# Kernel optimization log

Measured on AMD Instinct MI355X. Metric: run time of the kernel, lower is better.

The kernel has to match this reference:

```python
import jax, jax.numpy as jnp
import numpy as np

N, E, C, L = 50000, 800000, 64, 3  # nodes, edges, channels, message-passing layers
EPS = 1e-5  # torch.nn.LayerNorm default eps


def _mlp(h, W0, b0, W1, b1, W2, b2, g, beta):
    # MLP(input, hidden=[C, C], output=C) with ReLU between linears, LayerNorm at end
    h = jax.nn.relu(h @ W0 + b0)
    h = jax.nn.relu(h @ W1 + b1)
    h = h @ W2 + b2
    mu = jnp.mean(h, axis=-1, keepdims=True)
    var = jnp.var(h, axis=-1, keepdims=True)
    return (h - mu) * jax.lax.rsqrt(var + EPS) * g + beta


def setup_inputs() -> dict:
    key = jax.random.key(0)
    ks = jax.random.split(key, 12)
    def w(k, shape, fan_in):
        return (jax.random.normal(k, shape, jnp.float32) / np.float32(np.sqrt(fan_in)))
    return {
        "x": jax.random.normal(ks[0], (N, C), jnp.float32),
        "e": jax.random.normal(ks[1], (E, C), jnp.float32),
        "edge_index": jax.random.randint(ks[2], (2, E), 0, N),
        # edge_updater MLP params, stacked over L layers
        "ew0": w(ks[3], (L, 3 * C, C), 3 * C), "eb0": jnp.zeros((L, C), jnp.float32),
        "ew1": w(ks[4], (L, C, C), C),         "eb1": jnp.zeros((L, C), jnp.float32),
        "ew2": w(ks[5], (L, C, C), C),         "eb2": jnp.zeros((L, C), jnp.float32),
        "eg": jnp.ones((L, C), jnp.float32),   "ebt": jnp.zeros((L, C), jnp.float32),
        # node_updater MLP params
        "nw0": w(ks[6], (L, 2 * C, C), 2 * C), "nb0": jnp.zeros((L, C), jnp.float32),
        "nw1": w(ks[7], (L, C, C), C),         "nb1": jnp.zeros((L, C), jnp.float32),
        "nw2": w(ks[8], (L, C, C), C),         "nb2": jnp.zeros((L, C), jnp.float32),
        "ng": jnp.ones((L, C), jnp.float32),   "nbt": jnp.zeros((L, C), jnp.float32),
    }


def reference(x, e, edge_index, ew0, eb0, ew1, eb1, ew2, eb2, eg, ebt,
              nw0, nb0, nw1, nb1, nw2, nb2, ng, nbt):
    src, dst = edge_index[0], edge_index[1]
    for i in range(L):
        # e += edge_updater(cat(x_src, x_dst, e))
        e = e + _mlp(jnp.concatenate([x[src], x[dst], e], axis=1),
                     ew0[i], eb0[i], ew1[i], eb1[i], ew2[i], eb2[i], eg[i], ebt[i])
        # EdgeAggregation(aggr='add'): scatter-add edge features at target nodes
        agg = jax.ops.segment_sum(e, dst, num_segments=N)
        # x += node_updater(cat(x, agg))
        x = x + _mlp(jnp.concatenate([x, agg], axis=1),
                     nw0[i], nb0[i], nw1[i], nb1[i], nw2[i], nb2[i], ng[i], nbt[i])
    return (x, e)
```

## Files before the change

### kernel.cpp

```cpp
#include <hip/hip_runtime.h>

#define CH 64

using bf16x8 = __attribute__((ext_vector_type(8))) short;
using f32x4  = __attribute__((ext_vector_type(4))) float;

__device__ __forceinline__ unsigned short f2bf(float f) {
  unsigned int u = __float_as_uint(f);
  u = (u + 0x7FFFu + ((u >> 16) & 1u)) >> 16;
  return (unsigned short)u;
}

#define E0S 200
#define S64 72
#define N0S 136

#define EW0_L 0
#define EW1_L 12800
#define EW2_L 17408
#define EW_TOT 22016
#define EH0_L 22016
#define EH1_L 34816
#define E_LDS 39424

#define NW0_L 0
#define NW1_L 8704
#define NW2_L 13312
#define NW_TOT 17920
#define NH0_L 17920
#define NH1_L 26624
#define N_LDS 31232

#define WS_NW 66048
#define WS_AGG_B    262144
#define WS_ROWPTR_B 13062144
#define WS_NEXT_B   13262208
#define WS_EID_B    13462208

__global__ void prep_w(const float* __restrict__ ew0, const float* __restrict__ ew1,
                       const float* __restrict__ ew2, const float* __restrict__ nw0,
                       const float* __restrict__ nw1, const float* __restrict__ nw2,
                       unsigned short* __restrict__ ws) {
  int i = blockIdx.x * 256 + threadIdx.x;
  if (i < 36864) {
    int l = i / 12288, r = i % 12288, k = r / 64, n = r % 64;
    ws[l * EW_TOT + EW0_L + n * E0S + k] = f2bf(ew0[i]);
  } else if (i < 49152) {
    int j = i - 36864, l = j / 4096, r = j % 4096, k = r / 64, n = r % 64;
    ws[l * EW_TOT + EW1_L + n * S64 + k] = f2bf(ew1[j]);
  } else if (i < 61440) {
    int j = i - 49152, l = j / 4096, r = j % 4096, k = r / 64, n = r % 64;
    ws[l * EW_TOT + EW2_L + n * S64 + k] = f2bf(ew2[j]);
  } else if (i < 86016) {
    int j = i - 61440, l = j / 8192, r = j % 8192, k = r / 64, n = r % 64;
    ws[WS_NW + l * NW_TOT + NW0_L + n * N0S + k] = f2bf(nw0[j]);
  } else if (i < 98304) {
    int j = i - 86016, l = j / 4096, r = j % 4096, k = r / 64, n = r % 64;
    ws[WS_NW + l * NW_TOT + NW1_L + n * S64 + k] = f2bf(nw1[j]);
  } else if (i < 110592) {
    int j = i - 98304, l = j / 4096, r = j % 4096, k = r / 64, n = r % 64;
    ws[WS_NW + l * NW_TOT + NW2_L + n * S64 + k] = f2bf(nw2[j]);
  }
}

__global__ void hist_k(const int* __restrict__ dst, int* __restrict__ counts, int nE) {
  int i = blockIdx.x * 256 + threadIdx.x;
  if (i < nE) atomicAdd(counts + dst[i], 1);
}

__global__ void scan_k(const int* __restrict__ counts, int* __restrict__ row_ptr,
                       int* __restrict__ next, int n) {
  __shared__ int wsum[16];
  __shared__ int chunk_tot;
  __shared__ int base_sh;
  const int tid = threadIdx.x, lane = tid & 63, wv = tid >> 6;
  if (tid == 0) { base_sh = 0; row_ptr[0] = 0; }
  __syncthreads();
  for (int start = 0; start < n; start += 4096) {
    int idx = start + tid * 4;
    int v[4], s = 0;
#pragma unroll
    for (int k = 0; k < 4; ++k) { v[k] = (idx + k < n) ? counts[idx + k] : 0; s += v[k]; }
    int incl = s;
#pragma unroll
    for (int off = 1; off < 64; off <<= 1) {
      int t = __shfl_up(incl, off, 64);
      if (lane >= off) incl += t;
    }
    if (lane == 63) wsum[wv] = incl;
    __syncthreads();
    if (wv == 0 && lane < 16) {
      int w = wsum[lane];
      int wincl = w;
#pragma unroll
      for (int off = 1; off < 16; off <<= 1) {
        int t = __shfl_up(wincl, off, 16);
        if (lane >= off) wincl += t;
      }
      if (lane == 15) chunk_tot = wincl;
      wsum[lane] = wincl - w;
    }
    __syncthreads();
    int run = base_sh + wsum[wv] + (incl - s);
#pragma unroll
    for (int k = 0; k < 4; ++k) {
      int i = idx + k;
      if (i < n) { next[i] = run; run += v[k]; row_ptr[i + 1] = run; }
    }
    __syncthreads();
    if (tid == 0) base_sh += chunk_tot;
    __syncthreads();
  }
}

__global__ void scatter_k(const int* __restrict__ dst, int* __restrict__ next,
                          int* __restrict__ eid, int nE) {
  int i = blockIdx.x * 256 + threadIdx.x;
  if (i < nE) {
    int p = atomicAdd(next + dst[i], 1);
    eid[p] = i;
  }
}

__global__ __launch_bounds__(256, 2)
void edge_kernel(const float* x, const float* e_in, float* e_out,
                 const int* __restrict__ src, const int* __restrict__ dst,
                 const unsigned short* __restrict__ wg,
                 const float* __restrict__ b0, const float* __restrict__ b1,
                 const float* __restrict__ b2, const float* __restrict__ gam,
                 const float* __restrict__ bet, int nE) {
  __shared__ unsigned short lds[E_LDS];
  const int tid = threadIdx.x;
  {
    const uint4* s = (const uint4*)wg;
    uint4* d4 = (uint4*)lds;
    for (int i = tid; i < EW_TOT / 8; i += 256) d4[i] = s[i];
  }
  __syncthreads();

  const int wave = tid >> 6, lane = tid & 63;
  const int quad = lane >> 4, l15 = lane & 15;
  const int h0o = EH0_L + wave * 3200;
  const int h1o = EH1_L + wave * 1152;

  float b0c[4], b1c[4], b2c[4], gc[4], btc[4];
#pragma unroll
  for (int j = 0; j < 4; ++j) {
    int col = j * 16 + l15;
    b0c[j] = b0[col]; b1c[j] = b1[col]; b2c[j] = b2[col];
    gc[j] = gam[col]; btc[j] = bet[col];
  }

  for (int base = blockIdx.x * 64; base < nE; base += gridDim.x * 64) {
    const int ebase = base + wave * 16;
#pragma unroll
    for (int p = 0; p < 4; ++p) {
      int el = p * 4 + quad;
      int eidx = ebase + el;
      int s = src[eidx], d = dst[eidx];
      float4 vs = *(const float4*)(x + (size_t)s * CH + l15 * 4);
      float4 vd = *(const float4*)(x + (size_t)d * CH + l15 * 4);
      float4 ve = *(const float4*)(e_in + (size_t)eidx * CH + l15 * 4);
      ushort4 us; us.x = f2bf(vs.x); us.y = f2bf(vs.y); us.z = f2bf(vs.z); us.w = f2bf(vs.w);
      ushort4 ud; ud.x = f2bf(vd.x); ud.y = f2bf(vd.y); ud.z = f2bf(vd.z); ud.w = f2bf(vd.w);
      ushort4 ue; ue.x = f2bf(ve.x); ue.y = f2bf(ve.y); ue.z = f2bf(ve.z); ue.w = f2bf(ve.w);
      *(ushort4*)(lds + h0o + el * E0S + l15 * 4)       = us;
      *(ushort4*)(lds + h0o + el * E0S + 64 + l15 * 4)  = ud;
      *(ushort4*)(lds + h0o + el * E0S + 128 + l15 * 4) = ue;
    }
    f32x4 acc0[4];
#pragma unroll
    for (int j = 0; j < 4; ++j) acc0[j] = (f32x4){0.f, 0.f, 0.f, 0.f};
#pragma unroll
    for (int t = 0; t < 6; ++t) {
      bf16x8 a = *(const bf16x8*)(lds + h0o + l15 * E0S + t * 32 + quad * 8);
#pragma unroll
      for (int j = 0; j < 4; ++j) {
        bf16x8 b = *(const bf16x8*)(lds + EW0_L + (j * 16 + l15) * E0S + t * 32 + quad * 8);
        acc0[j] = __builtin_amdgcn_mfma_f32_16x16x32_bf16(a, b, acc0[j], 0, 0, 0);
      }
    }
#pragma unroll
    for (int j = 0; j < 4; ++j) {
      int col = j * 16 + l15;
#pragma unroll
      for (int r = 0; r < 4; ++r) {
        float v = fmaxf(acc0[j][r] + b0c[j], 0.f);
        lds[h1o + (quad * 4 + r) * S64 + col] = f2bf(v);
      }
    }
    f32x4 acc1[4];
#pragma unroll
    for (int j = 0; j < 4; ++j) acc1[j] = (f32x4){0.f, 0.f, 0.f, 0.f};
#pragma unroll
    for (int t = 0; t < 2; ++t) {
      bf16x8 a = *(const bf16x8*)(lds + h1o + l15 * S64 + t * 32 + quad * 8);
#pragma unroll
      for (int j = 0; j < 4; ++j) {
        bf16x8 b = *(const bf16x8*)(lds + EW1_L + (j * 16 + l15) * S64 + t * 32 + quad * 8);
        acc1[j] = __builtin_amdgcn_mfma_f32_16x16x32_bf16(a, b, acc1[j], 0, 0, 0);
      }
    }
#pragma unroll
    for (int j = 0; j < 4; ++j) {
      int col = j * 16 + l15;
#pragma unroll
      for (int r = 0; r < 4; ++r) {
        float v = fmaxf(acc1[j][r] + b1c[j], 0.f);
        lds[h0o + (quad * 4 + r) * S64 + col] = f2bf(v);
      }
    }
    f32x4 acc2[4];
#pragma unroll
    for (int j = 0; j < 4; ++j) acc2[j] = (f32x4){0.f, 0.f, 0.f, 0.f};
#pragma unroll
    for (int t = 0; t < 2; ++t) {
      bf16x8 a = *(const bf16x8*)(lds + h0o + l15 * S64 + t * 32 + quad * 8);
#pragma unroll
      for (int j = 0; j < 4; ++j) {
        bf16x8 b = *(const bf16x8*)(lds + EW2_L + (j * 16 + l15) * S64 + t * 32 + quad * 8);
        acc2[j] = __builtin_amdgcn_mfma_f32_16x16x32_bf16(a, b, acc2[j], 0, 0, 0);
      }
    }
    float vv[4][4], s1[4], s2[4];
#pragma unroll
    for (int r = 0; r < 4; ++r) { s1[r] = 0.f; s2[r] = 0.f; }
#pragma unroll
    for (int j = 0; j < 4; ++j)
#pragma unroll
      for (int r = 0; r < 4; ++r) {
        float v = acc2[j][r] + b2c[j];
        vv[j][r] = v; s1[r] += v; s2[r] += v * v;
      }
#pragma unroll
    for (int m = 1; m < 16; m <<= 1)
#pragma unroll
      for (int r = 0; r < 4; ++r) {
        s1[r] += __shfl_xor(s1[r], m, 64);
        s2[r] += __shfl_xor(s2[r], m, 64);
      }
#pragma unroll
    for (int r = 0; r < 4; ++r) {
      int eidx = ebase + quad * 4 + r;
      float mean = s1[r] * 0.015625f;
      float var = s2[r] * 0.015625f - mean * mean;
      float rstd = rsqrtf(var + 1e-5f);
      const float* ein_row = e_in + (size_t)eidx * CH;
      float* eout_row = e_out + (size_t)eidx * CH;
#pragma unroll
      for (int j = 0; j < 4; ++j) {
        int col = j * 16 + l15;
        float y = (vv[j][r] - mean) * rstd * gc[j] + btc[j];
        eout_row[col] = ein_row[col] + y;
      }
    }
  }
}

__global__ __launch_bounds__(256)
void agg_kernel(const float* __restrict__ e, const int* __restrict__ row_ptr,
                const int* __restrict__ eid, float* __restrict__ agg, int nN) {
  int node = blockIdx.x * 4 + (threadIdx.x >> 6);
  int lane = threadIdx.x & 63;
  if (node >= nN) return;
  int r0 = row_ptr[node], r1 = row_ptr[node + 1];
  float s0 = 0.f, s1 = 0.f, s2 = 0.f, s3 = 0.f;
  int i = r0;
  for (; i + 4 <= r1; i += 4) {
    int e0 = eid[i], e1 = eid[i + 1], e2 = eid[i + 2], e3 = eid[i + 3];
    s0 += e[(size_t)e0 * CH + lane];
    s1 += e[(size_t)e1 * CH + lane];
    s2 += e[(size_t)e2 * CH + lane];
    s3 += e[(size_t)e3 * CH + lane];
  }
  for (; i < r1; ++i) s0 += e[(size_t)eid[i] * CH + lane];
  agg[(size_t)node * CH + lane] = (s0 + s1) + (s2 + s3);
}

__global__ __launch_bounds__(256, 2)
void node_kernel(const float* x_in, const float* __restrict__ agg_in,
                 const unsigned short* __restrict__ wg,
                 const float* __restrict__ b0, const float* __restrict__ b1,
                 const float* __restrict__ b2, const float* __restrict__ gam,
                 const float* __restrict__ bet, float* x_out, int nN) {
  __shared__ unsigned short lds[N_LDS];
  const int tid = threadIdx.x;
  {
    const uint4* s = (const uint4*)wg;
    uint4* d4 = (uint4*)lds;
    for (int i = tid; i < NW_TOT / 8; i += 256) d4[i] = s[i];
  }
  __syncthreads();

  const int wave = tid >> 6, lane = tid & 63;
  const int quad = lane >> 4, l15 = lane & 15;
  const int nbase = (blockIdx.x * 4 + wave) * 16;
  if (nbase >= nN) return;
  const int h0o = NH0_L + wave * 2176;
  const int h1o = NH1_L + wave * 1152;

  float b0c[4], b1c[4], b2c[4], gc[4], btc[4];
#pragma unroll
  for (int j = 0; j < 4; ++j) {
    int col = j * 16 + l15;
    b0c[j] = b0[col]; b1c[j] = b1[col]; b2c[j] = b2[col];
    gc[j] = gam[col]; btc[j] = bet[col];
  }

#pragma unroll
  for (int p = 0; p < 4; ++p) {
    int nl = p * 4 + quad;
    int node = nbase + nl;
    float4 vx = *(const float4*)(x_in + (size_t)node * CH + l15 * 4);
    float4 va = *(const float4*)(agg_in + (size_t)node * CH + l15 * 4);
    ushort4 ux; ux.x = f2bf(vx.x); ux.y = f2bf(vx.y); ux.z = f2bf(vx.z); ux.w = f2bf(vx.w);
    ushort4 ua; ua.x = f2bf(va.x); ua.y = f2bf(va.y); ua.z = f2bf(va.z); ua.w = f2bf(va.w);
    *(ushort4*)(lds + h0o + nl * N0S + l15 * 4)      = ux;
    *(ushort4*)(lds + h0o + nl * N0S + 64 + l15 * 4) = ua;
  }
  f32x4 acc0[4];
#pragma unroll
  for (int j = 0; j < 4; ++j) acc0[j] = (f32x4){0.f, 0.f, 0.f, 0.f};
#pragma unroll
  for (int t = 0; t < 4; ++t) {
    bf16x8 a = *(const bf16x8*)(lds + h0o + l15 * N0S + t * 32 + quad * 8);
#pragma unroll
    for (int j = 0; j < 4; ++j) {
      bf16x8 b = *(const bf16x8*)(lds + NW0_L + (j * 16 + l15) * N0S + t * 32 + quad * 8);
      acc0[j] = __builtin_amdgcn_mfma_f32_16x16x32_bf16(a, b, acc0[j], 0, 0, 0);
    }
  }
#pragma unroll
  for (int j = 0; j < 4; ++j) {
    int col = j * 16 + l15;
#pragma unroll
    for (int r = 0; r < 4; ++r) {
      float v = fmaxf(acc0[j][r] + b0c[j], 0.f);
      lds[h1o + (quad * 4 + r) * S64 + col] = f2bf(v);
    }
  }
  f32x4 acc1[4];
#pragma unroll
  for (int j = 0; j < 4; ++j) acc1[j] = (f32x4){0.f, 0.f, 0.f, 0.f};
#pragma unroll
  for (int t = 0; t < 2; ++t) {
    bf16x8 a = *(const bf16x8*)(lds + h1o + l15 * S64 + t * 32 + quad * 8);
#pragma unroll
    for (int j = 0; j < 4; ++j) {
      bf16x8 b = *(const bf16x8*)(lds + NW1_L + (j * 16 + l15) * S64 + t * 32 + quad * 8);
      acc1[j] = __builtin_amdgcn_mfma_f32_16x16x32_bf16(a, b, acc1[j], 0, 0, 0);
    }
  }
#pragma unroll
  for (int j = 0; j < 4; ++j) {
    int col = j * 16 + l15;
#pragma unroll
    for (int r = 0; r < 4; ++r) {
      float v = fmaxf(acc1[j][r] + b1c[j], 0.f);
      lds[h0o + (quad * 4 + r) * S64 + col] = f2bf(v);
    }
  }
  f32x4 acc2[4];
#pragma unroll
  for (int j = 0; j < 4; ++j) acc2[j] = (f32x4){0.f, 0.f, 0.f, 0.f};
#pragma unroll
  for (int t = 0; t < 2; ++t) {
    bf16x8 a = *(const bf16x8*)(lds + h0o + l15 * S64 + t * 32 + quad * 8);
#pragma unroll
    for (int j = 0; j < 4; ++j) {
      bf16x8 b = *(const bf16x8*)(lds + NW2_L + (j * 16 + l15) * S64 + t * 32 + quad * 8);
      acc2[j] = __builtin_amdgcn_mfma_f32_16x16x32_bf16(a, b, acc2[j], 0, 0, 0);
    }
  }
  float vv[4][4], s1[4], s2[4];
#pragma unroll
  for (int r = 0; r < 4; ++r) { s1[r] = 0.f; s2[r] = 0.f; }
#pragma unroll
  for (int j = 0; j < 4; ++j)
#pragma unroll
    for (int r = 0; r < 4; ++r) {
      float v = acc2[j][r] + b2c[j];
      vv[j][r] = v; s1[r] += v; s2[r] += v * v;
    }
#pragma unroll
  for (int m = 1; m < 16; m <<= 1)
#pragma unroll
    for (int r = 0; r < 4; ++r) {
      s1[r] += __shfl_xor(s1[r], m, 64);
      s2[r] += __shfl_xor(s2[r], m, 64);
    }
#pragma unroll
  for (int r = 0; r < 4; ++r) {
    int node = nbase + quad * 4 + r;
    float mean = s1[r] * 0.015625f;
    float var = s2[r] * 0.015625f - mean * mean;
    float rstd = rsqrtf(var + 1e-5f);
    const float* xin_row = x_in + (size_t)node * CH;
    float* xout_row = x_out + (size_t)node * CH;
#pragma unroll
    for (int j = 0; j < 4; ++j) {
      int col = j * 16 + l15;
      float y = (vv[j][r] - mean) * rstd * gc[j] + btc[j];
      xout_row[col] = xin_row[col] + y;
    }
  }
}

extern "C" void kernel_launch(void* const* d_in, const int* in_sizes, int n_in,
                              void* d_out, int out_size, void* d_ws, size_t ws_size,
                              hipStream_t stream) {
  const float* x0 = (const float*)d_in[0];
  const float* e0 = (const float*)d_in[1];
  const int* ei  = (const int*)d_in[2];
  const float* ew0 = (const float*)d_in[3];
  const float* eb0 = (const float*)d_in[4];
  const float* ew1 = (const float*)d_in[5];
  const float* eb1 = (const float*)d_in[6];
  const float* ew2 = (const float*)d_in[7];
  const float* eb2 = (const float*)d_in[8];
  const float* eg  = (const float*)d_in[9];
  const float* ebt = (const float*)d_in[10];
  const float* nw0 = (const float*)d_in[11];
  const float* nb0 = (const float*)d_in[12];
  const float* nw1 = (const float*)d_in[13];
  const float* nb1 = (const float*)d_in[14];
  const float* nw2 = (const float*)d_in[15];
  const float* nb2 = (const float*)d_in[16];
  const float* ng  = (const float*)d_in[17];
  const float* nbt = (const float*)d_in[18];

  const int N = in_sizes[0] / CH;
  const int E = in_sizes[1] / CH;
  const int* src = ei;
  const int* dst = ei + E;

  float* xout = (float*)d_out;
  float* eout = (float*)d_out + (size_t)N * CH;

  unsigned short* wsu = (unsigned short*)d_ws;
  float* agg    = (float*)((char*)d_ws + WS_AGG_B);
  int* row_ptr  = (int*)((char*)d_ws + WS_ROWPTR_B);
  int* nxt      = (int*)((char*)d_ws + WS_NEXT_B);
  int* eid      = (int*)((char*)d_ws + WS_EID_B);

  prep_w<<<432, 256, 0, stream>>>(ew0, ew1, ew2, nw0, nw1, nw2, wsu);

  hipMemsetAsync(nxt, 0, (size_t)N * sizeof(int), stream);
  hist_k<<<(E + 255) / 256, 256, 0, stream>>>(dst, nxt, E);
  scan_k<<<1, 1024, 0, stream>>>(nxt, row_ptr, nxt, N);
  scatter_k<<<(E + 255) / 256, 256, 0, stream>>>(dst, nxt, eid, E);

  for (int l = 0; l < 3; ++l) {
    const float* xin = (l == 0) ? x0 : xout;
    const float* einp = (l == 0) ? e0 : eout;
    edge_kernel<<<512, 256, 0, stream>>>(
        xin, einp, eout, src, dst, wsu + l * EW_TOT,
        eb0 + l * CH, eb1 + l * CH, eb2 + l * CH, eg + l * CH, ebt + l * CH, E);
    agg_kernel<<<(N + 3) / 4, 256, 0, stream>>>(eout, row_ptr, eid, agg, N);
    node_kernel<<<(N / 16 + 3) / 4, 256, 0, stream>>>(
        xin, agg, wsu + WS_NW + l * NW_TOT,
        nb0 + l * CH, nb1 + l * CH, nb2 + l * CH, ng + l * CH, nbt + l * CH,
        xout, N);
  }
}
```

Before: 1.136 ms.

## Load MLP inputs directly into MFMA registers, vectorize aggregation, persistent node kernel

Edge and node kernels now load gathered x/e rows directly into bf16 MFMA A-fragments in registers, removing the LDS staging buffer and shrinking LDS use. The edge kernel uses 512-thread blocks processing 128 edges per iteration, and the node kernel becomes a grid-stride loop over a fixed grid. The aggregation kernel splits a node's edges across four lane groups using float4 loads and reduces with shuffles. This raises occupancy and cuts LDS traffic, at the cost of more register pressure and less coalesced per-lane global loads.

Result: faster. 1.056 ms (-7.0%).

```diff
diff --git a/kernel.cpp b/kernel.cpp
--- a/kernel.cpp
+++ b/kernel.cpp
@@ -11,6 +11,15 @@
   return (unsigned short)u;
 }
 
+__device__ __forceinline__ bf16x8 pack8(f32x4 a, f32x4 b) {
+  bf16x8 r;
+  r[0] = (short)f2bf(a[0]); r[1] = (short)f2bf(a[1]);
+  r[2] = (short)f2bf(a[2]); r[3] = (short)f2bf(a[3]);
+  r[4] = (short)f2bf(b[0]); r[5] = (short)f2bf(b[1]);
+  r[6] = (short)f2bf(b[2]); r[7] = (short)f2bf(b[3]);
+  return r;
+}
+
 #define E0S 200
 #define S64 72
 #define N0S 136
@@ -19,17 +28,13 @@
 #define EW1_L 12800
 #define EW2_L 17408
 #define EW_TOT 22016
-#define EH0_L 22016
-#define EH1_L 34816
-#define E_LDS 39424
+#define E_LDS 31232
 
 #define NW0_L 0
 #define NW1_L 8704
 #define NW2_L 13312
 #define NW_TOT 17920
-#define NH0_L 17920
-#define NH1_L 26624
-#define N_LDS 31232
+#define N_LDS 22528
 
 #define WS_NW 66048
 #define WS_AGG_B    262144
@@ -122,8 +127,8 @@
   }
 }
 
-__global__ __launch_bounds__(256, 2)
-void edge_kernel(const float* x, const float* e_in, float* e_out,
+__global__ __launch_bounds__(512, 4)
+void edge_kernel(const float* __restrict__ x, const float* e_in, float* e_out,
                  const int* __restrict__ src, const int* __restrict__ dst,
                  const unsigned short* __restrict__ wg,
                  const float* __restrict__ b0, const float* __restrict__ b1,
@@ -132,16 +137,15 @@
   __shared__ unsigned short lds[E_LDS];
   const int tid = threadIdx.x;
   {
-    const uint4* s = (const uint4*)wg;
+    const uint4* s4 = (const uint4*)wg;
     uint4* d4 = (uint4*)lds;
-    for (int i = tid; i < EW_TOT / 8; i += 256) d4[i] = s[i];
+    for (int i = tid; i < EW_TOT / 8; i += 512) d4[i] = s4[i];
   }
   __syncthreads();
 
   const int wave = tid >> 6, lane = tid & 63;
   const int quad = lane >> 4, l15 = lane & 15;
-  const int h0o = EH0_L + wave * 3200;
-  const int h1o = EH1_L + wave * 1152;
+  const int h1o = EW_TOT + wave * 1152;
 
   float b0c[4], b1c[4], b2c[4], gc[4], btc[4];
 #pragma unroll
@@ -151,33 +155,47 @@
     gc[j] = gam[col]; btc[j] = bet[col];
   }
 
-  for (int base = blockIdx.x * 64; base < nE; base += gridDim.x * 64) {
+  const int o1 = quad * 8, o2 = 32 + quad * 8;
+
+  for (int base = blockIdx.x * 128; base < nE; base += gridDim.x * 128) {
     const int ebase = base + wave * 16;
-#pragma unroll
-    for (int p = 0; p < 4; ++p) {
-      int el = p * 4 + quad;
-      int eidx = ebase + el;
-      int s = src[eidx], d = dst[eidx];
-      float4 vs = *(const float4*)(x + (size_t)s * CH + l15 * 4);
-      float4 vd = *(const float4*)(x + (size_t)d * CH + l15 * 4);
-      float4 ve = *(const float4*)(e_in + (size_t)eidx * CH + l15 * 4);
-      ushort4 us; us.x = f2bf(vs.x); us.y = f2bf(vs.y); us.z = f2bf(vs.z); us.w = f2bf(vs.w);
-      ushort4 ud; ud.x = f2bf(vd.x); ud.y = f2bf(vd.y); ud.z = f2bf(vd.z); ud.w = f2bf(vd.w);
-      ushort4 ue; ue.x = f2bf(ve.x); ue.y = f2bf(ve.y); ue.z = f2bf(ve.z); ue.w = f2bf(ve.w);
-      *(ushort4*)(lds + h0o + el * E0S + l15 * 4)       = us;
-      *(ushort4*)(lds + h0o + el * E0S + 64 + l15 * 4)  = ud;
-      *(ushort4*)(lds + h0o + el * E0S + 128 + l15 * 4) = ue;
-    }
+    const int row = ebase + l15;
+    int si = src[row], di = dst[row];
+    const float* xs = x + (size_t)si * CH;
+    const float* xd = x + (size_t)di * CH;
+    const float* er = e_in + (size_t)row * CH;
+    bf16x8 af[6];
+    {
+      f32x4 a0 = *(const f32x4*)(xs + o1);
+      f32x4 a1 = *(const f32x4*)(xs + o1 + 4);
+      f32x4 a2 = *(const f32x4*)(xs + o2);
+      f32x4 a3 = *(const f32x4*)(xs + o2 + 4);
+      af[0] = pack8(a0, a1); af[1] = pack8(a2, a3);
+    }
+    {
+      f32x4 a0 = *(const f32x4*)(xd + o1);
+      f32x4 a1 = *(const f32x4*)(xd + o1 + 4);
+      f32x4 a2 = *(const f32x4*)(xd + o2);
+      f32x4 a3 = *(const f32x4*)(xd + o2 + 4);
+      af[2] = pack8(a0, a1); af[3] = pack8(a2, a3);
+    }
+    {
+      f32x4 a0 = *(const f32x4*)(er + o1);
+      f32x4 a1 = *(const f32x4*)(er + o1 + 4);
+      f32x4 a2 = *(const f32x4*)(er + o2);
+      f32x4 a3 = *(const f32x4*)(er + o2 + 4);
+      af[4] = pack8(a0, a1); af[5] = pack8(a2, a3);
+    }
+
     f32x4 acc0[4];
 #pragma unroll
     for (int j = 0; j < 4; ++j) acc0[j] = (f32x4){0.f, 0.f, 0.f, 0.f};
 #pragma unroll
     for (int t = 0; t < 6; ++t) {
-      bf16x8 a = *(const bf16x8*)(lds + h0o + l15 * E0S + t * 32 + quad * 8);
 #pragma unroll
       for (int j = 0; j < 4; ++j) {
         bf16x8 b = *(const bf16x8*)(lds + EW0_L + (j * 16 + l15) * E0S + t * 32 + quad * 8);
-        acc0[j] = __builtin_amdgcn_mfma_f32_16x16x32_bf16(a, b, acc0[j], 0, 0, 0);
+        acc0[j] = __builtin_amdgcn_mfma_f32_16x16x32_bf16(af[t], b, acc0[j], 0, 0, 0);
       }
     }
 #pragma unroll
@@ -207,7 +225,7 @@
 #pragma unroll
       for (int r = 0; r < 4; ++r) {
         float v = fmaxf(acc1[j][r] + b1c[j], 0.f);
-        lds[h0o + (quad * 4 + r) * S64 + col] = f2bf(v);
+        lds[h1o + (quad * 4 + r) * S64 + col] = f2bf(v);
       }
     }
     f32x4 acc2[4];
@@ -215,7 +233,7 @@
     for (int j = 0; j < 4; ++j) acc2[j] = (f32x4){0.f, 0.f, 0.f, 0.f};
 #pragma unroll
     for (int t = 0; t < 2; ++t) {
-      bf16x8 a = *(const bf16x8*)(lds + h0o + l15 * S64 + t * 32 + quad * 8);
+      bf16x8 a = *(const bf16x8*)(lds + h1o + l15 * S64 + t * 32 + quad * 8);
 #pragma unroll
       for (int j = 0; j < 4; ++j) {
         bf16x8 b = *(const bf16x8*)(lds + EW2_L + (j * 16 + l15) * S64 + t * 32 + quad * 8);
@@ -261,23 +279,33 @@
 void agg_kernel(const float* __restrict__ e, const int* __restrict__ row_ptr,
                 const int* __restrict__ eid, float* __restrict__ agg, int nN) {
   int node = blockIdx.x * 4 + (threadIdx.x >> 6);
+  if (node >= nN) return;
   int lane = threadIdx.x & 63;
-  if (node >= nN) return;
+  int quad = lane >> 4, l15 = lane & 15;
   int r0 = row_ptr[node], r1 = row_ptr[node + 1];
-  float s0 = 0.f, s1 = 0.f, s2 = 0.f, s3 = 0.f;
-  int i = r0;
-  for (; i + 4 <= r1; i += 4) {
-    int e0 = eid[i], e1 = eid[i + 1], e2 = eid[i + 2], e3 = eid[i + 3];
-    s0 += e[(size_t)e0 * CH + lane];
-    s1 += e[(size_t)e1 * CH + lane];
-    s2 += e[(size_t)e2 * CH + lane];
-    s3 += e[(size_t)e3 * CH + lane];
-  }
-  for (; i < r1; ++i) s0 += e[(size_t)eid[i] * CH + lane];
-  agg[(size_t)node * CH + lane] = (s0 + s1) + (s2 + s3);
-}
-
-__global__ __launch_bounds__(256, 2)
+  f32x4 s = (f32x4){0.f, 0.f, 0.f, 0.f};
+  f32x4 s2 = (f32x4){0.f, 0.f, 0.f, 0.f};
+  int i = r0 + quad;
+  for (; i + 4 < r1; i += 8) {
+    int e0 = eid[i], e1 = eid[i + 4];
+    f32x4 a = *(const f32x4*)(e + (size_t)e0 * CH + l15 * 4);
+    f32x4 b = *(const f32x4*)(e + (size_t)e1 * CH + l15 * 4);
+    s += a; s2 += b;
+  }
+  for (; i < r1; i += 4) {
+    int e0 = eid[i];
+    s += *(const f32x4*)(e + (size_t)e0 * CH + l15 * 4);
+  }
+  s += s2;
+#pragma unroll
+  for (int c = 0; c < 4; ++c) {
+    s[c] += __shfl_xor(s[c], 16, 64);
+    s[c] += __shfl_xor(s[c], 32, 64);
+  }
+  if (quad == 0) *(f32x4*)(agg + (size_t)node * CH + l15 * 4) = s;
+}
+
+__global__ __launch_bounds__(256, 3)
 void node_kernel(const float* x_in, const float* __restrict__ agg_in,
                  const unsigned short* __restrict__ wg,
                  const float* __restrict__ b0, const float* __restrict__ b1,
@@ -286,18 +314,15 @@
   __shared__ unsigned short lds[N_LDS];
   const int tid = threadIdx.x;
   {
-    const uint4* s = (const uint4*)wg;
+    const uint4* s4 = (const uint4*)wg;
     uint4* d4 = (uint4*)lds;
-    for (int i = tid; i < NW_TOT / 8; i += 256) d4[i] = s[i];
+    for (int i = tid; i < NW_TOT / 8; i += 256) d4[i] = s4[i];
   }
   __syncthreads();
 
   const int wave = tid >> 6, lane = tid & 63;
   const int quad = lane >> 4, l15 = lane & 15;
-  const int nbase = (blockIdx.x * 4 + wave) * 16;
-  if (nbase >= nN) return;
-  const int h0o = NH0_L + wave * 2176;
-  const int h1o = NH1_L + wave * 1152;
+  const int h1o = NW_TOT + wave * 1152;
 
   float b0c[4], b1c[4], b2c[4], gc[4], btc[4];
 #pragma unroll
@@ -307,101 +332,114 @@
     gc[j] = gam[col]; btc[j] = bet[col];
   }
 
-#pragma unroll
-  for (int p = 0; p < 4; ++p) {
-    int nl = p * 4 + quad;
-    int node = nbase + nl;
-    float4 vx = *(const float4*)(x_in + (size_t)node * CH + l15 * 4);
-    float4 va = *(const float4*)(agg_in + (size_t)node * CH + l15 * 4);
-    ushort4 ux; ux.x = f2bf(vx.x); ux.y = f2bf(vx.y); ux.z = f2bf(vx.z); ux.w = f2bf(vx.w);
-    ushort4 ua; ua.x = f2bf(va.x); ua.y = f2bf(va.y); ua.z = f2bf(va.z); ua.w = f2bf(va.w);
-    *(ushort4*)(lds + h0o + nl * N0S + l15 * 4)      = ux;
-    *(ushort4*)(lds + h0o + nl * N0S + 64 + l15 * 4) = ua;
-  }
-  f32x4 acc0[4];
-#pragma unroll
-  for (int j = 0; j < 4; ++j) acc0[j] = (f32x4){0.f, 0.f, 0.f, 0.f};
-#pragma unroll
-  for (int t = 0; t < 4; ++t) {
-    bf16x8 a = *(const bf16x8*)(lds + h0o + l15 * N0S + t * 32 + quad * 8);
-#pragma unroll
-    for (int j = 0; j < 4; ++j) {
-      bf16x8 b = *(const bf16x8*)(lds + NW0_L + (j * 16 + l15) * N0S + t * 32 + quad * 8);
-      acc0[j] = __builtin_amdgcn_mfma_f32_16x16x32_bf16(a, b, acc0[j], 0, 0, 0);
-    }
-  }
-#pragma unroll
-  for (int j = 0; j < 4; ++j) {
-    int col = j * 16 + l15;
-#pragma unroll
-    for (int r = 0; r < 4; ++r) {
-      float v = fmaxf(acc0[j][r] + b0c[j], 0.f);
-      lds[h1o + (quad * 4 + r) * S64 + col] = f2bf(v);
-    }
-  }
-  f32x4 acc1[4];
-#pragma unroll
-  for (int j = 0; j < 4; ++j) acc1[j] = (f32x4){0.f, 0.f, 0.f, 0.f};
-#pragma unroll
-  for (int t = 0; t < 2; ++t) {
-    bf16x8 a = *(const bf16x8*)(lds + h1o + l15 * S64 + t * 32 + quad * 8);
-#pragma unroll
-    for (int j = 0; j < 4; ++j) {
-      bf16x8 b = *(const bf16x8*)(lds + NW1_L + (j * 16 + l15) * S64 + t * 32 + quad * 8);
-      acc1[j] = __builtin_amdgcn_mfma_f32_16x16x32_bf16(a, b, acc1[j], 0, 0, 0);
-    }
-  }
-#pragma unroll
-  for (int j = 0; j < 4; ++j) {
-    int col = j * 16 + l15;
-#pragma unroll
-    for (int r = 0; r < 4; ++r) {
-      float v = fmaxf(acc1[j][r] + b1c[j], 0.f);
-      lds[h0o + (quad * 4 + r) * S64 + col] = f2bf(v);
-    }
-  }
-  f32x4 acc2[4];
-#pragma unroll
-  for (int j = 0; j < 4; ++j) acc2[j] = (f32x4){0.f, 0.f, 0.f, 0.f};
-#pragma unroll
-  for (int t = 0; t < 2; ++t) {
-    bf16x8 a = *(const bf16x8*)(lds + h0o + l15 * S64 + t * 32 + quad * 8);
-#pragma unroll
-    for (int j = 0; j < 4; ++j) {
-      bf16x8 b = *(const bf16x8*)(lds + NW2_L + (j * 16 + l15) * S64 + t * 32 + quad * 8);
-      acc2[j] = __builtin_amdgcn_mfma_f32_16x16x32_bf16(a, b, acc2[j], 0, 0, 0);
-    }
-  }
-  float vv[4][4], s1[4], s2[4];
-#pragma unroll
-  for (int r = 0; r < 4; ++r) { s1[r] = 0.f; s2[r] = 0.f; }
-#pragma unroll
-  for (int j = 0; j < 4; ++j)
-#pragma unroll
-    for (int r = 0; r < 4; ++r) {
-      float v = acc2[j][r] + b2c[j];
-      vv[j][r] = v; s1[r] += v; s2[r] += v * v;
-    }
-#pragma unroll
-  for (int m = 1; m < 16; m <<= 1)
-#pragma unroll
-    for (int r = 0; r < 4; ++r) {
-      s1[r] += __shfl_xor(s1[r], m, 64);
-      s2[r] += __shfl_xor(s2[r], m, 64);
-    }
-#pragma unroll
-  for (int r = 0; r < 4; ++r) {
-    int node = nbase + quad * 4 + r;
-    float mean = s1[r] * 0.015625f;
-    float var = s2[r] * 0.015625f - mean * mean;
-    float rstd = rsqrtf(var + 1e-5f);
-    const float* xin_row = x_in + (size_t)node * CH;
-    float* xout_row = x_out + (size_t)node * CH;
+  const int o1 = quad * 8, o2 = 32 + quad * 8;
+
+  for (int base = blockIdx.x * 64; base < nN; base += gridDim.x * 64) {
+    const int nbase = base + wave * 16;
+    if (nbase >= nN) continue;
+    const int row = nbase + l15;
+    const float* xr = x_in + (size_t)row * CH;
+    const float* ar = agg_in + (size_t)row * CH;
+    bf16x8 af[4];
+    {
+      f32x4 a0 = *(const f32x4*)(xr + o1);
+      f32x4 a1 = *(const f32x4*)(xr + o1 + 4);
+      f32x4 a2 = *(const f32x4*)(xr + o2);
+      f32x4 a3 = *(const f32x4*)(xr + o2 + 4);
+      af[0] = pack8(a0, a1); af[1] = pack8(a2, a3);
+    }
+    {
+      f32x4 a0 = *(const f32x4*)(ar + o1);
+      f32x4 a1 = *(const f32x4*)(ar + o1 + 4);
+      f32x4 a2 = *(const f32x4*)(ar + o2);
+      f32x4 a3 = *(const f32x4*)(ar + o2 + 4);
+      af[2] = pack8(a0, a1); af[3] = pack8(a2, a3);
+    }
+
+    f32x4 acc0[4];
+#pragma unroll
+    for (int j = 0; j < 4; ++j) acc0[j] = (f32x4){0.f, 0.f, 0.f, 0.f};
+#pragma unroll
+    for (int t = 0; t < 4; ++t) {
+#pragma unroll
+      for (int j = 0; j < 4; ++j) {
+        bf16x8 b = *(const bf16x8*)(lds + NW0_L + (j * 16 + l15) * N0S + t * 32 + quad * 8);
+        acc0[j] = __builtin_amdgcn_mfma_f32_16x16x32_bf16(af[t], b, acc0[j], 0, 0, 0);
+      }
+    }
 #pragma unroll
     for (int j = 0; j < 4; ++j) {
       int col = j * 16 + l15;
-      float y = (vv[j][r] - mean) * rstd * gc[j] + btc[j];
-      xout_row[col] = xin_row[col] + y;
+#pragma unroll
+      for (int r = 0; r < 4; ++r) {
+        float v = fmaxf(acc0[j][r] + b0c[j], 0.f);
+        lds[h1o + (quad * 4 + r) * S64 + col] = f2bf(v);
+      }
+    }
+    f32x4 acc1[4];
+#pragma unroll
+    for (int j = 0; j < 4; ++j) acc1[j] = (f32x4){0.f, 0.f, 0.f, 0.f};
+#pragma unroll
+    for (int t = 0; t < 2; ++t) {
+      bf16x8 a = *(const bf16x8*)(lds + h1o + l15 * S64 + t * 32 + quad * 8);
+#pragma unroll
+      for (int j = 0; j < 4; ++j) {
+        bf16x8 b = *(const bf16x8*)(lds + NW1_L + (j * 16 + l15) * S64 + t * 32 + quad * 8);
+        acc1[j] = __builtin_amdgcn_mfma_f32_16x16x32_bf16(a, b, acc1[j], 0, 0, 0);
+      }
+    }
+#pragma unroll
+    for (int j = 0; j < 4; ++j) {
+      int col = j * 16 + l15;
+#pragma unroll
+      for (int r = 0; r < 4; ++r) {
+        float v = fmaxf(acc1[j][r] + b1c[j], 0.f);
+        lds[h1o + (quad * 4 + r) * S64 + col] = f2bf(v);
+      }
+    }
+    f32x4 acc2[4];
+#pragma unroll
+    for (int j = 0; j < 4; ++j) acc2[j] = (f32x4){0.f, 0.f, 0.f, 0.f};
+#pragma unroll
+    for (int t = 0; t < 2; ++t) {
+      bf16x8 a = *(const bf16x8*)(lds + h1o + l15 * S64 + t * 32 + quad * 8);
+#pragma unroll
+      for (int j = 0; j < 4; ++j) {
+        bf16x8 b = *(const bf16x8*)(lds + NW2_L + (j * 16 + l15) * S64 + t * 32 + quad * 8);
+        acc2[j] = __builtin_amdgcn_mfma_f32_16x16x32_bf16(a, b, acc2[j], 0, 0, 0);
+      }
+    }
+    float vv[4][4], s1[4], s2[4];
+#pragma unroll
+    for (int r = 0; r < 4; ++r) { s1[r] = 0.f; s2[r] = 0.f; }
+#pragma unroll
+    for (int j = 0; j < 4; ++j)
+#pragma unroll
+      for (int r = 0; r < 4; ++r) {
+        float v = acc2[j][r] + b2c[j];
+        vv[j][r] = v; s1[r] += v; s2[r] += v * v;
+      }
+#pragma unroll
+    for (int m = 1; m < 16; m <<= 1)
+#pragma unroll
+      for (int r = 0; r < 4; ++r) {
+        s1[r] += __shfl_xor(s1[r], m, 64);
+        s2[r] += __shfl_xor(s2[r], m, 64);
+      }
+#pragma unroll
+    for (int r = 0; r < 4; ++r) {
+      int node = nbase + quad * 4 + r;
+      float mean = s1[r] * 0.015625f;
+      float var = s2[r] * 0.015625f - mean * mean;
+      float rstd = rsqrtf(var + 1e-5f);
+      const float* xin_row = x_in + (size_t)node * CH;
+      float* xout_row = x_out + (size_t)node * CH;
+#pragma unroll
+      for (int j = 0; j < 4; ++j) {
+        int col = j * 16 + l15;
+        float y = (vv[j][r] - mean) * rstd * gc[j] + btc[j];
+        xout_row[col] = xin_row[col] + y;
+      }
     }
   }
 }
@@ -453,11 +491,11 @@
   for (int l = 0; l < 3; ++l) {
     const float* xin = (l == 0) ? x0 : xout;
     const float* einp = (l == 0) ? e0 : eout;
-    edge_kernel<<<512, 256, 0, stream>>>(
+    edge_kernel<<<512, 512, 0, stream>>>(
         xin, einp, eout, src, dst, wsu + l * EW_TOT,
         eb0 + l * CH, eb1 + l * CH, eb2 + l * CH, eg + l * CH, ebt + l * CH, E);
     agg_kernel<<<(N + 3) / 4, 256, 0, stream>>>(eout, row_ptr, eid, agg, N);
-    node_kernel<<<(N / 16 + 3) / 4, 256, 0, stream>>>(
+    node_kernel<<<768, 256, 0, stream>>>(
         xin, agg, wsu + WS_NW + l * NW_TOT,
         nb0 + l * CH, nb1 + l * CH, nb2 + l * CH, ng + l * CH, nbt + l * CH,
         xout, N);
```
